# Kernel tuning notes

Hardware: AMD Instinct MI355X
Metric: run time of the kernel (lower is better)

Reference implementation:

```python
import jax, jax.numpy as jnp
import numpy as np

N, F_DIM, H, K, T = 4096, 256, 256, 3, 5
START, END = 10, 3  # args.len_numerical_features, args.num_class


def setup_inputs() -> dict:
    key = jax.random.key(0)
    ks = jax.random.split(key, 8)
    s = 0.05
    x = jax.random.normal(ks[0], (N, F_DIM), dtype=jnp.float32)
    adj = jax.random.randint(ks[1], (N, N, K), 0, 2, dtype=jnp.int32)
    gnn_w = jax.random.normal(ks[2], (K, F_DIM, H), dtype=jnp.float32) * s
    gnn_b = jnp.zeros((K, H), dtype=jnp.float32)
    w_ih = jax.random.normal(ks[3], (K, 4 * H, H), dtype=jnp.float32) * s
    w_hh = jax.random.normal(ks[4], (K, 4 * H, H), dtype=jnp.float32) * s
    b_ih = jnp.zeros((K, 4 * H), dtype=jnp.float32)
    b_hh = jnp.zeros((K, 4 * H), dtype=jnp.float32)
    fc_w = jax.random.normal(ks[5], (K, F_DIM, H), dtype=jnp.float32) * s
    fc_b = jnp.zeros((K, F_DIM), dtype=jnp.float32)
    return dict(x=x, gnn_w=gnn_w, gnn_b=gnn_b, w_ih=w_ih, w_hh=w_hh,
                b_ih=b_ih, b_hh=b_hh, fc_w=fc_w, fc_b=fc_b, adj=adj)


def _gcn(x, a_bin, w, b):
    # PyG GCNConv: A_hat = A + I (self-loops added on top of existing edges,
    # weight 1), out = D^-1/2 A_hat D^-1/2 (x @ W) + b
    a = a_bin + jnp.eye(N, dtype=x.dtype)
    deg = a.sum(axis=1)
    dinv = jnp.where(deg > 0, jax.lax.rsqrt(deg), 0.0)
    a_norm = dinv[:, None] * a * dinv[None, :]
    return a_norm @ (x @ w) + b


def _lstm_last(xt, w_ih, w_hh, b_ih, b_hh):
    # batch_first LSTM over T identical inputs xt [N,H]; returns h at last step
    def step(carry, _):
        h, c = carry
        g = xt @ w_ih.T + b_ih + h @ w_hh.T + b_hh
        i, f, gg, o = jnp.split(g, 4, axis=-1)  # torch gate order: i, f, g, o
        c = jax.nn.sigmoid(f) * c + jax.nn.sigmoid(i) * jnp.tanh(gg)
        h = jax.nn.sigmoid(o) * jnp.tanh(c)
        return (h, c), None
    zero = jnp.zeros((xt.shape[0], H), dtype=xt.dtype)
    (h, c), _ = jax.lax.scan(step, (zero, zero), None, length=T)
    return h


def _sig_slice(z):
    return z.at[:, START:F_DIM - END].set(jax.nn.sigmoid(z[:, START:F_DIM - END]))


def reference(x, gnn_w, gnn_b, w_ih, w_hh, b_ih, b_hh, fc_w, fc_b, adj):
    deltas, zbars = [], []
    for k in range(K):
        a_bin = (adj[:, :, k] != 0).astype(x.dtype)
        # GCN output is identical across timesteps -> compute once
        gnn_out = _gcn(x, a_bin, gnn_w[k], gnn_b[k])
        h_last = _lstm_last(gnn_out, w_ih[k], w_hh[k], b_ih[k], b_hh[k])
        delta = jnp.tanh(h_last @ fc_w[k].T + fc_b[k])  # [N, F]
        deltas.append(delta)
        zbars.append(_sig_slice(x + delta))
    delta_z = jnp.stack(deltas, -1).mean(-1)
    res_z_bar = jnp.stack(zbars, -1)  # [N, F, K]
    pred_matrix = _sig_slice(x + delta_z)
    return pred_matrix, res_z_bar, adj
```

## Files before the change

### kernel.cpp

```cpp
#include <hip/hip_runtime.h>
#include <stdint.h>

#define NN_ 4096
#define FD 256
#define HD 256
#define KC 3
#define GD 1024
#define SA 40
#define BPITCH 144

typedef __attribute__((ext_vector_type(4))) unsigned int vu4;
typedef __attribute__((ext_vector_type(4))) int vi4;
typedef __attribute__((ext_vector_type(4))) float vf4;
typedef __attribute__((ext_vector_type(4))) unsigned short vus4;
typedef __attribute__((ext_vector_type(8))) short short8;
typedef __attribute__((ext_vector_type(4))) float f32x4;

typedef __attribute__((address_space(1))) const void GV;
typedef __attribute__((address_space(3))) void LV;
__device__ __forceinline__ void gl16(const void* g, void* l) {
    __builtin_amdgcn_global_load_lds((GV*)g, (LV*)l, 16, 0, 0);
}

__device__ __forceinline__ float b2f(unsigned short u) {
    unsigned int v = ((unsigned int)u) << 16; float f; __builtin_memcpy(&f, &v, 4); return f;
}
__device__ __forceinline__ unsigned short f2b(float x) {
    unsigned int u; __builtin_memcpy(&u, &x, 4);
    u = (u + 0x7FFFu + ((u >> 16) & 1u)) >> 16;
    return (unsigned short)u;
}
__device__ __forceinline__ void cvt8(const float* __restrict__ g, unsigned short* o) {
    vf4 a = *(const vf4*)g, b = *(const vf4*)(g + 4);
    o[0] = f2b(a[0]); o[1] = f2b(a[1]); o[2] = f2b(a[2]); o[3] = f2b(a[3]);
    o[4] = f2b(b[0]); o[5] = f2b(b[1]); o[6] = f2b(b[2]); o[7] = f2b(b[3]);
}
__device__ __forceinline__ float sigm(float v) { return 1.f / (1.f + __expf(-v)); }

__global__ __launch_bounds__(256) void adj_pass(const int* __restrict__ adj,
        float* __restrict__ adj_out, unsigned char* __restrict__ abits,
        float* __restrict__ dinv,
        const float* __restrict__ wih, const float* __restrict__ whh,
        const float* __restrict__ fcw, unsigned short* __restrict__ wb) {
    const int i = blockIdx.x, t = threadIdx.x;
    if (i < 864) {
        size_t e = ((size_t)i * 256 + t) * 8;
        const float* src; size_t off;
        if (e < 786432)       { src = wih; off = e; }
        else if (e < 1572864) { src = whh; off = e - 786432; }
        else                  { src = fcw; off = e - 1572864; }
        alignas(16) unsigned short o[8];
        cvt8(src + off, o);
        *(vu4*)(wb + e) = *(vu4*)o;
    }
    __shared__ unsigned char nib[3][1024];
    __shared__ float r0[256], r1[256], r2[256];
    const int* src = adj + (size_t)i * 12288;
    float* dstf = adj_out + (size_t)i * 12288;
    float s0 = 0.f, s1 = 0.f, s2 = 0.f;
#pragma unroll
    for (int it = 0; it < 4; ++it) {
        int p = it * 256 + t;
        int jq = p * 4;
        vi4 a = *(const vi4*)(src + jq * 3);
        vi4 b = *(const vi4*)(src + jq * 3 + 4);
        vi4 c = *(const vi4*)(src + jq * 3 + 8);
        int vv[12] = {a[0],a[1],a[2],a[3],b[0],b[1],b[2],b[3],c[0],c[1],c[2],c[3]};
        float ff[12];
#pragma unroll
        for (int e = 0; e < 12; ++e) ff[e] = vv[e] ? 1.f : 0.f;
        vf4 w0 = {ff[0],ff[1],ff[2],ff[3]}, w1 = {ff[4],ff[5],ff[6],ff[7]}, w2 = {ff[8],ff[9],ff[10],ff[11]};
        *(vf4*)(dstf + jq * 3) = w0; *(vf4*)(dstf + jq * 3 + 4) = w1; *(vf4*)(dstf + jq * 3 + 8) = w2;
#pragma unroll
        for (int k = 0; k < 3; ++k) {
            unsigned int nb = (vv[k] ? 1u : 0u) | (vv[3 + k] ? 2u : 0u)
                            | (vv[6 + k] ? 4u : 0u) | (vv[9 + k] ? 8u : 0u);
            nib[k][p] = (unsigned char)nb;
        }
        s0 += ff[0] + ff[3] + ff[6] + ff[9];
        s1 += ff[1] + ff[4] + ff[7] + ff[10];
        s2 += ff[2] + ff[5] + ff[8] + ff[11];
    }
    r0[t] = s0; r1[t] = s1; r2[t] = s2;
    __syncthreads();
#pragma unroll
    for (int k = 0; k < 3; ++k) {
        unsigned int b0 = (unsigned int)nib[k][t * 4 + 0] | ((unsigned int)nib[k][t * 4 + 1] << 4);
        unsigned int b1 = (unsigned int)nib[k][t * 4 + 2] | ((unsigned int)nib[k][t * 4 + 3] << 4);
        *(unsigned short*)(abits + ((size_t)k * NN_ + i) * 512 + t * 2) =
            (unsigned short)(b0 | (b1 << 8));
    }
    for (int off = 128; off > 0; off >>= 1) {
        if (t < off) { r0[t] += r0[t + off]; r1[t] += r1[t + off]; r2[t] += r2[t + off]; }
        __syncthreads();
    }
    if (t == 0) {
        dinv[i]            = 1.f / sqrtf(1.f + r0[0]);
        dinv[NN_ + i]      = 1.f / sqrtf(1.f + r1[0]);
        dinv[2 * NN_ + i]  = 1.f / sqrtf(1.f + r2[0]);
    }
}

__global__ __launch_bounds__(256) void gemm_xw(const float* __restrict__ x,
        const float* __restrict__ gw, const float* __restrict__ dinv,
        unsigned short* __restrict__ yT) {
    __shared__ __align__(16) unsigned short sA[64 * SA], sB[64 * SA];
    const int bi = blockIdx.x, bj = blockIdx.y, k = blockIdx.z;
    const int t = threadIdx.x, lane = t & 63, wave = t >> 6;
    const int m = lane & 15, q = lane >> 4, ko = q * 8;
    const int h0 = bj * 64;
    f32x4 acc[4] = {};
    const float* A0 = x + (size_t)(bi * 64) * FD;
    const float* B0 = gw + (size_t)k * FD * HD;
    const int r = t >> 2, c8 = (t & 3) << 3;
    const int fB = t >> 3, c8B = (t & 7) << 3;
    for (int k0 = 0; k0 < FD; k0 += 32) {
        alignas(16) unsigned short tA[8], tB[8];
        cvt8(A0 + (size_t)r * FD + k0 + c8, tA);
        *(vu4*)(sA + r * SA + c8) = *(vu4*)tA;
        cvt8(B0 + (size_t)(k0 + fB) * HD + h0 + c8B, tB);
#pragma unroll
        for (int e = 0; e < 8; ++e) sB[(c8B + e) * SA + fB] = tB[e];
        __syncthreads();
        short8 af = *(const short8*)(sA + (wave * 16 + m) * SA + ko);
#pragma unroll
        for (int ct = 0; ct < 4; ++ct) {
            short8 bf = *(const short8*)(sB + (ct * 16 + m) * SA + ko);
            acc[ct] = __builtin_amdgcn_mfma_f32_16x16x32_bf16(af, bf, acc[ct], 0, 0, 0);
        }
        __syncthreads();
    }
    unsigned short* yTk = yT + (size_t)k * HD * NN_;
#pragma unroll
    for (int ct = 0; ct < 4; ++ct)
#pragma unroll
        for (int r2 = 0; r2 < 4; ++r2) {
            int col = h0 + ct * 16 + m;
            int row = bi * 64 + wave * 16 + q * 4 + r2;
            yTk[(size_t)col * NN_ + row] = f2b(acc[ct][r2] * dinv[(size_t)k * NN_ + row]);
        }
}

__global__ __launch_bounds__(256) void gemm_agg(const unsigned char* __restrict__ abits,
        const unsigned short* __restrict__ yT, unsigned short* __restrict__ pbuf) {
    __shared__ __align__(16) unsigned char bitsA[128 * BPITCH];
    __shared__ __align__(16) unsigned short sB[128 * 32];
    const int d = blockIdx.x;
    const int w = (d & 7) * 96 + (d >> 3);
    const int bh = w & 1, bi = (w >> 1) & 31, z = w >> 6;
    const int k = z >> 2, s = z & 3;
    const int t = threadIdx.x, lane = t & 63, wave = t >> 6;
    const int wi = wave & 1, wh = wave >> 1;
    const int m = lane & 15, q = lane >> 4, ko = q * 8;
    const int i0 = bi * 128, h0 = bh * 128, jbase = s * 1024;
    {
        const int row = t >> 1, half = t & 1;
        const unsigned char* bsrc = abits + ((size_t)k * NN_ + i0 + row) * 512 + s * 128 + half * 64;
        unsigned char* bdst = bitsA + row * BPITCH + half * 64;
        vu4 v0 = *(const vu4*)(bsrc);
        vu4 v1 = *(const vu4*)(bsrc + 16);
        vu4 v2 = *(const vu4*)(bsrc + 32);
        vu4 v3 = *(const vu4*)(bsrc + 48);
        *(vu4*)(bdst)      = v0;
        *(vu4*)(bdst + 16) = v1;
        *(vu4*)(bdst + 32) = v2;
        *(vu4*)(bdst + 48) = v3;
    }
    f32x4 acc[4][4] = {};
    const int lrow = lane >> 2, lcol = (lane & 3) << 3;
    const unsigned short* Bg0 = yT + ((size_t)(k * 256 + h0 + wave * 32 + lrow)) * NN_ + jbase + lcol;
    const unsigned short* Bg1 = Bg0 + (size_t)16 * NN_;
    unsigned short* lB0 = sB + (wave * 32) * 32;
    unsigned short* lB1 = lB0 + 16 * 32;
    const int arow = (wi * 64 + m) * BPITCH + q;
    for (int j0 = 0; j0 < 1024; j0 += 32) {
        gl16(Bg0 + j0, lB0);
        gl16(Bg1 + j0, lB1);
        __syncthreads();
        const int jby = j0 >> 3;
        short8 af[4], bf[4];
#pragma unroll
        for (int rt = 0; rt < 4; ++rt) {
            unsigned int by = bitsA[arow + rt * 16 * BPITCH + jby];
#pragma unroll
            for (int e = 0; e < 8; ++e)
                af[rt][e] = (short)(((by >> e) & 1u) ? (short)0x3F80 : (short)0);
        }
#pragma unroll
        for (int ct = 0; ct < 4; ++ct)
            bf[ct] = *(const short8*)(sB + (wh * 64 + ct * 16 + m) * 32 + ko);
#pragma unroll
        for (int ct = 0; ct < 4; ++ct)
#pragma unroll
            for (int rt = 0; rt < 4; ++rt)
                acc[rt][ct] = __builtin_amdgcn_mfma_f32_16x16x32_bf16(af[rt], bf[ct], acc[rt][ct], 0, 0, 0);
        __syncthreads();
    }
    const int addself = ((bi >> 3) == s);
#pragma unroll
    for (int rt = 0; rt < 4; ++rt)
#pragma unroll
        for (int ct = 0; ct < 4; ++ct)
#pragma unroll
            for (int r2 = 0; r2 < 4; ++r2) {
                int row = i0 + wi * 64 + rt * 16 + q * 4 + r2;
                int col = h0 + wh * 64 + ct * 16 + m;
                float v = acc[rt][ct][r2];
                if (addself) v += b2f(yT[((size_t)k * 256 + col) * NN_ + row]);
                pbuf[(((size_t)s * 3 + k) * NN_ + row) * 256 + col] = f2b(v);
            }
}

__global__ __launch_bounds__(256) void agg_reduce(const unsigned short* __restrict__ pbuf,
        const float* __restrict__ dinv, const float* __restrict__ gnnb,
        unsigned short* __restrict__ xt) {
    size_t e8 = ((size_t)blockIdx.x * 256 + threadIdx.x) * 8;
    int k = (int)(e8 >> 20);
    int i = (int)((e8 >> 8) & 4095);
    int h = (int)(e8 & 255);
    float di = dinv[k * NN_ + i];
    const size_t KIH = (size_t)KC * NN_ * HD;
    alignas(16) unsigned short p0[8], p1[8], p2[8], p3[8], o[8];
    *(vu4*)p0 = *(const vu4*)(pbuf + 0 * KIH + e8);
    *(vu4*)p1 = *(const vu4*)(pbuf + 1 * KIH + e8);
    *(vu4*)p2 = *(const vu4*)(pbuf + 2 * KIH + e8);
    *(vu4*)p3 = *(const vu4*)(pbuf + 3 * KIH + e8);
#pragma unroll
    for (int e = 0; e < 8; ++e) {
        float v = b2f(p0[e]) + b2f(p1[e]) + b2f(p2[e]) + b2f(p3[e]);
        o[e] = f2b(di * v + gnnb[k * HD + h + e]);
    }
    *(vu4*)(xt + e8) = *(vu4*)o;
}

__global__ __launch_bounds__(256) void lstm_mm(const unsigned short* __restrict__ A,
        const unsigned short* __restrict__ W, const float* __restrict__ b1,
        const float* __restrict__ b2, unsigned short* __restrict__ gX2,
        float* __restrict__ cbuf, unsigned short* __restrict__ hbuf, int mode) {
    __shared__ __align__(16) unsigned short sA[128 * 32];
    __shared__ __align__(16) unsigned short sB[128 * 32];
    const int d = blockIdx.x;
    const int w = (d & 7) * 96 + (d >> 3);
    const int chb = w & 7, bn = w >> 3;
    const int t = threadIdx.x, lane = t & 63, wave = t >> 6;
    const int m = lane & 15, q = lane >> 4, ko = q * 8;
    const int kk = bn >> 5;
    f32x4 acc[2][2][4] = {};
    const int lrow = lane >> 2, lcol = (lane & 3) << 3;
    const unsigned short* A0 = A + (size_t)bn * 128 * 256;
    const unsigned short* W0 = W + (size_t)kk * GD * 256 + (size_t)chb * 32 * 256;
    const unsigned short* Ag0 = A0 + (size_t)(wave * 32 + lrow) * 256 + lcol;
    const unsigned short* Ag1 = Ag0 + 16 * 256;
    const unsigned short* Bg0 = W0 + (size_t)(wave * 256 + lrow) * 256 + lcol;
    const unsigned short* Bg1 = Bg0 + 16 * 256;
    unsigned short* lA0 = sA + (wave * 32) * 32;
    unsigned short* lA1 = lA0 + 16 * 32;
    unsigned short* lB0 = sB + (wave * 32) * 32;
    unsigned short* lB1 = lB0 + 16 * 32;
    for (int k0 = 0; k0 < 256; k0 += 32) {
        gl16(Ag0 + k0, lA0);
        gl16(Ag1 + k0, lA1);
        gl16(Bg0 + k0, lB0);
        gl16(Bg1 + k0, lB1);
        __syncthreads();
        short8 af[2];
#pragma unroll
        for (int rt = 0; rt < 2; ++rt)
            af[rt] = *(const short8*)(sA + (wave * 32 + rt * 16 + m) * 32 + ko);
#pragma unroll
        for (int g = 0; g < 4; ++g)
#pragma unroll
            for (int cc = 0; cc < 2; ++cc) {
                short8 bf = *(const short8*)(sB + (g * 32 + cc * 16 + m) * 32 + ko);
#pragma unroll
                for (int rt = 0; rt < 2; ++rt)
                    acc[rt][cc][g] = __builtin_amdgcn_mfma_f32_16x16x32_bf16(af[rt], bf, acc[rt][cc][g], 0, 0, 0);
            }
        __syncthreads();
    }
#pragma unroll
    for (int rt = 0; rt < 2; ++rt)
#pragma unroll
        for (int cc = 0; cc < 2; ++cc)
#pragma unroll
            for (int r2 = 0; r2 < 4; ++r2) {
                int row = bn * 128 + wave * 32 + rt * 16 + q * 4 + r2;
                int ch = chb * 32 + cc * 16 + m;
                size_t goff = ((size_t)row * 256 + ch) * 4;
                size_t coff = (size_t)row * 256 + ch;
                if (mode == 0) {
                    float v[4];
                    vus4 o;
#pragma unroll
                    for (int g = 0; g < 4; ++g) {
                        v[g] = acc[rt][cc][g][r2]
                             + b1[kk * GD + g * 256 + ch] + b2[kk * GD + g * 256 + ch];
                        o[g] = f2b(v[g]);
                    }
                    *(vus4*)(gX2 + goff) = o;
                    float cn = sigm(v[0]) * tanhf(v[2]);
                    cbuf[coff] = cn;
                    hbuf[coff] = f2b(sigm(v[3]) * tanhf(cn));
                } else {
                    vus4 gv = *(const vus4*)(gX2 + goff);
                    float iv = acc[rt][cc][0][r2] + b2f(gv[0]);
                    float fv = acc[rt][cc][1][r2] + b2f(gv[1]);
                    float gg = acc[rt][cc][2][r2] + b2f(gv[2]);
                    float ov = acc[rt][cc][3][r2] + b2f(gv[3]);
                    float cn = sigm(fv) * cbuf[coff] + sigm(iv) * tanhf(gg);
                    cbuf[coff] = cn;
                    hbuf[coff] = f2b(sigm(ov) * tanhf(cn));
                }
            }
}

__global__ __launch_bounds__(256) void fc_final(const unsigned short* __restrict__ A,
        const unsigned short* __restrict__ W, const float* __restrict__ fcb,
        const float* __restrict__ x, float* __restrict__ pred, float* __restrict__ res) {
    __shared__ __align__(16) unsigned short sA[3][64 * 32], sB[3][64 * 32];
    const int bg = blockIdx.x, bn = blockIdx.y;
    const int t = threadIdx.x, lane = t & 63, wave = t >> 6;
    const int m = lane & 15, q = lane >> 4, ko = q * 8;
    f32x4 acc[3][4] = {};
    const int lrow = lane >> 2, lcol = (lane & 3) << 3;
    const unsigned short* Ag[3]; const unsigned short* Bg[3];
#pragma unroll
    for (int k = 0; k < 3; ++k) {
        Ag[k] = A + ((size_t)k * NN_ + bn * 64 + wave * 16 + lrow) * HD + lcol;
        Bg[k] = W + ((size_t)k * FD + bg * 64 + wave * 16 + lrow) * HD + lcol;
    }
    for (int k0 = 0; k0 < HD; k0 += 32) {
#pragma unroll
        for (int k = 0; k < 3; ++k) {
            gl16(Ag[k] + k0, sA[k] + (wave * 16) * 32);
            gl16(Bg[k] + k0, sB[k] + (wave * 16) * 32);
        }
        __syncthreads();
#pragma unroll
        for (int k = 0; k < 3; ++k) {
            short8 af = *(const short8*)(sA[k] + (wave * 16 + m) * 32 + ko);
#pragma unroll
            for (int ct = 0; ct < 4; ++ct) {
                short8 bf = *(const short8*)(sB[k] + (ct * 16 + m) * 32 + ko);
                acc[k][ct] = __builtin_amdgcn_mfma_f32_16x16x32_bf16(af, bf, acc[k][ct], 0, 0, 0);
            }
        }
        __syncthreads();
    }
#pragma unroll
    for (int ct = 0; ct < 4; ++ct)
#pragma unroll
        for (int r2 = 0; r2 < 4; ++r2) {
            int col = bg * 64 + ct * 16 + m;
            int row = bn * 64 + wave * 16 + q * 4 + r2;
            float d0 = tanhf(acc[0][ct][r2] + fcb[col]);
            float d1 = tanhf(acc[1][ct][r2] + fcb[FD + col]);
            float d2 = tanhf(acc[2][ct][r2] + fcb[2 * FD + col]);
            float xf = x[(size_t)row * FD + col];
            bool sg = (col >= 10) && (col < 253);
            float dm = (d0 + d1 + d2) * (1.f / 3.f);
            float p = xf + dm; if (sg) p = sigm(p);
            pred[(size_t)row * FD + col] = p;
            float z0 = xf + d0; if (sg) z0 = sigm(z0);
            float z1 = xf + d1; if (sg) z1 = sigm(z1);
            float z2 = xf + d2; if (sg) z2 = sigm(z2);
            size_t rb = ((size_t)row * FD + col) * 3;
            res[rb] = z0; res[rb + 1] = z1; res[rb + 2] = z2;
        }
}

extern "C" void kernel_launch(void* const* d_in, const int* in_sizes, int n_in,
                              void* d_out, int out_size, void* d_ws, size_t ws_size,
                              hipStream_t stream) {
    const float* x    = (const float*)d_in[0];
    const float* gnnw = (const float*)d_in[1];
    const float* gnnb = (const float*)d_in[2];
    const float* wih  = (const float*)d_in[3];
    const float* whh  = (const float*)d_in[4];
    const float* bih  = (const float*)d_in[5];
    const float* bhh  = (const float*)d_in[6];
    const float* fcw  = (const float*)d_in[7];
    const float* fcb  = (const float*)d_in[8];
    const int*   adj  = (const int*)d_in[9];

    float* out = (float*)d_out;
    float* out_pred = out;
    float* out_res  = out + (size_t)NN_ * FD;
    float* out_adj  = out + (size_t)NN_ * FD * 4;

    char* ws = (char*)d_ws;
    float*          dinv  = (float*)ws;
    unsigned short* R1    = (unsigned short*)(ws + 49152);
    unsigned short* R2    = (unsigned short*)(ws + 6340608);
    unsigned short* wb    = (unsigned short*)(ws + 12632064);
    unsigned short* pbuf  = (unsigned short*)(ws + 16171008);
    unsigned short* gX2   = pbuf;
    unsigned char*  abits = (unsigned char*)(ws + 41336832);
    float*          cbuf  = (float*)(ws + 47628288);
    const unsigned short* wihb = wb;
    const unsigned short* whhb = wb + 786432;
    const unsigned short* fcwb = wb + 1572864;
    (void)ws_size; (void)in_sizes; (void)n_in; (void)out_size;

    adj_pass<<<dim3(4096), 256, 0, stream>>>(adj, out_adj, abits, dinv, wih, whh, fcw, wb);
    gemm_xw<<<dim3(64, 4, 3), 256, 0, stream>>>(x, gnnw, dinv, R1 );
    gemm_agg<<<dim3(768), 256, 0, stream>>>(abits, R1 , pbuf);
    agg_reduce<<<dim3(1536), 256, 0, stream>>>(pbuf, dinv, gnnb, R2 );
    lstm_mm<<<dim3(768), 256, 0, stream>>>(R2 , wihb, bih, bhh, gX2, cbuf, R1 , 0);
    for (int tstep = 1; tstep < 5; ++tstep)
        lstm_mm<<<dim3(768), 256, 0, stream>>>(R1 , whhb, nullptr, nullptr, gX2, cbuf, R1 , 1);
    fc_final<<<dim3(4, 64), 256, 0, stream>>>(R1 , fcwb, fcb, x, out_pred, out_res);
}
```

Measured before the change: 586.8 us.

## Fuse aggregation reduce into first LSTM GEMM, pre-convert GEMM inputs, widen agg tiles

Folds the split-K partial-sum reduction, normalisation and bias into the A-tile load of the first LSTM input GEMM, which removes the separate agg_reduce kernel and its round trip through memory. x and the transposed GCN weight are converted to bf16 in the adjacency pass, so gemm_xw can use direct global-to-LDS loads. gemm_agg now covers all 256 hidden columns per block (384 blocks), so each adjacency bit tile is expanded once instead of twice, at the cost of higher register pressure. The LSTM steps ping-pong between two hidden buffers, and the workspace is re-laid out so gX2 no longer aliases pbuf.

```diff
diff --git a/kernel.cpp b/kernel.cpp
--- a/kernel.cpp
+++ b/kernel.cpp
@@ -6,7 +6,6 @@
 #define HD 256
 #define KC 3
 #define GD 1024
-#define SA 40
 #define BPITCH 144
 
 typedef __attribute__((ext_vector_type(4))) unsigned int vu4;
@@ -41,17 +40,35 @@
         float* __restrict__ adj_out, unsigned char* __restrict__ abits,
         float* __restrict__ dinv,
         const float* __restrict__ wih, const float* __restrict__ whh,
-        const float* __restrict__ fcw, unsigned short* __restrict__ wb) {
+        const float* __restrict__ fcw, unsigned short* __restrict__ wb,
+        const float* __restrict__ gnnw, const float* __restrict__ x,
+        unsigned short* __restrict__ gwT, unsigned short* __restrict__ xb) {
     const int i = blockIdx.x, t = threadIdx.x;
-    if (i < 864) {
+    if (i < 1472) {
         size_t e = ((size_t)i * 256 + t) * 8;
-        const float* src; size_t off;
-        if (e < 786432)       { src = wih; off = e; }
-        else if (e < 1572864) { src = whh; off = e - 786432; }
-        else                  { src = fcw; off = e - 1572864; }
-        alignas(16) unsigned short o[8];
-        cvt8(src + off, o);
-        *(vu4*)(wb + e) = *(vu4*)o;
+        if (e < 1769472) {
+            const float* src; size_t off;
+            if (e < 786432)       { src = wih; off = e; }
+            else if (e < 1572864) { src = whh; off = e - 786432; }
+            else                  { src = fcw; off = e - 1572864; }
+            alignas(16) unsigned short o[8];
+            cvt8(src + off, o);
+            *(vu4*)(wb + e) = *(vu4*)o;
+        } else if (e < 1966080) {
+            size_t idx = e - 1769472;
+            int k = (int)(idx >> 16), rem = (int)(idx & 65535);
+            int h = rem >> 8, f0 = rem & 255;
+            alignas(16) unsigned short o[8];
+#pragma unroll
+            for (int j = 0; j < 8; ++j)
+                o[j] = f2b(gnnw[((size_t)k * 256 + f0 + j) * 256 + h]);
+            *(vu4*)(gwT + idx) = *(vu4*)o;
+        } else {
+            size_t idx = e - 1966080;
+            alignas(16) unsigned short o[8];
+            cvt8(x + idx, o);
+            *(vu4*)(xb + idx) = *(vu4*)o;
+        }
     }
     __shared__ unsigned char nib[3][1024];
     __shared__ float r0[256], r1[256], r2[256];
@@ -101,31 +118,27 @@
     }
 }
 
-__global__ __launch_bounds__(256) void gemm_xw(const float* __restrict__ x,
-        const float* __restrict__ gw, const float* __restrict__ dinv,
+__global__ __launch_bounds__(256) void gemm_xw(const unsigned short* __restrict__ xb,
+        const unsigned short* __restrict__ gwT, const float* __restrict__ dinv,
         unsigned short* __restrict__ yT) {
-    __shared__ __align__(16) unsigned short sA[64 * SA], sB[64 * SA];
-    const int bi = blockIdx.x, bj = blockIdx.y, k = blockIdx.z;
+    __shared__ __align__(16) unsigned short sA[64 * 32], sB[64 * 32];
+    const int bg = blockIdx.x, bn = blockIdx.y, k = blockIdx.z;
     const int t = threadIdx.x, lane = t & 63, wave = t >> 6;
     const int m = lane & 15, q = lane >> 4, ko = q * 8;
-    const int h0 = bj * 64;
     f32x4 acc[4] = {};
-    const float* A0 = x + (size_t)(bi * 64) * FD;
-    const float* B0 = gw + (size_t)k * FD * HD;
-    const int r = t >> 2, c8 = (t & 3) << 3;
-    const int fB = t >> 3, c8B = (t & 7) << 3;
+    const int lrow = lane >> 2, lcol = (lane & 3) << 3;
+    const unsigned short* Ag = xb + (size_t)(bn * 64 + wave * 16 + lrow) * FD + lcol;
+    const unsigned short* Bg = gwT + (size_t)k * 65536 + (size_t)(bg * 64 + wave * 16 + lrow) * FD + lcol;
+    unsigned short* lA = sA + (wave * 16) * 32;
+    unsigned short* lB = sB + (wave * 16) * 32;
     for (int k0 = 0; k0 < FD; k0 += 32) {
-        alignas(16) unsigned short tA[8], tB[8];
-        cvt8(A0 + (size_t)r * FD + k0 + c8, tA);
-        *(vu4*)(sA + r * SA + c8) = *(vu4*)tA;
-        cvt8(B0 + (size_t)(k0 + fB) * HD + h0 + c8B, tB);
-#pragma unroll
-        for (int e = 0; e < 8; ++e) sB[(c8B + e) * SA + fB] = tB[e];
-        __syncthreads();
-        short8 af = *(const short8*)(sA + (wave * 16 + m) * SA + ko);
+        gl16(Ag + k0, lA);
+        gl16(Bg + k0, lB);
+        __syncthreads();
+        short8 af = *(const short8*)(sA + (wave * 16 + m) * 32 + ko);
 #pragma unroll
         for (int ct = 0; ct < 4; ++ct) {
-            short8 bf = *(const short8*)(sB + (ct * 16 + m) * SA + ko);
+            short8 bf = *(const short8*)(sB + (ct * 16 + m) * 32 + ko);
             acc[ct] = __builtin_amdgcn_mfma_f32_16x16x32_bf16(af, bf, acc[ct], 0, 0, 0);
         }
         __syncthreads();
@@ -135,8 +148,8 @@
     for (int ct = 0; ct < 4; ++ct)
 #pragma unroll
         for (int r2 = 0; r2 < 4; ++r2) {
-            int col = h0 + ct * 16 + m;
-            int row = bi * 64 + wave * 16 + q * 4 + r2;
+            int col = bg * 64 + ct * 16 + m;
+            int row = bn * 64 + wave * 16 + q * 4 + r2;
             yTk[(size_t)col * NN_ + row] = f2b(acc[ct][r2] * dinv[(size_t)k * NN_ + row]);
         }
 }
@@ -144,15 +157,15 @@
 __global__ __launch_bounds__(256) void gemm_agg(const unsigned char* __restrict__ abits,
         const unsigned short* __restrict__ yT, unsigned short* __restrict__ pbuf) {
     __shared__ __align__(16) unsigned char bitsA[128 * BPITCH];
-    __shared__ __align__(16) unsigned short sB[128 * 32];
+    __shared__ __align__(16) unsigned short sB[256 * 32];
     const int d = blockIdx.x;
-    const int w = (d & 7) * 96 + (d >> 3);
-    const int bh = w & 1, bi = (w >> 1) & 31, z = w >> 6;
+    const int w = (d & 7) * 48 + (d >> 3);
+    const int bi = w & 31, z = w >> 5;
     const int k = z >> 2, s = z & 3;
     const int t = threadIdx.x, lane = t & 63, wave = t >> 6;
     const int wi = wave & 1, wh = wave >> 1;
     const int m = lane & 15, q = lane >> 4, ko = q * 8;
-    const int i0 = bi * 128, h0 = bh * 128, jbase = s * 1024;
+    const int i0 = bi * 128, jbase = s * 1024;
     {
         const int row = t >> 1, half = t & 1;
         const unsigned char* bsrc = abits + ((size_t)k * NN_ + i0 + row) * 512 + s * 128 + half * 64;
@@ -166,77 +179,142 @@
         *(vu4*)(bdst + 32) = v2;
         *(vu4*)(bdst + 48) = v3;
     }
-    f32x4 acc[4][4] = {};
+    f32x4 acc[4][8] = {};
     const int lrow = lane >> 2, lcol = (lane & 3) << 3;
-    const unsigned short* Bg0 = yT + ((size_t)(k * 256 + h0 + wave * 32 + lrow)) * NN_ + jbase + lcol;
-    const unsigned short* Bg1 = Bg0 + (size_t)16 * NN_;
-    unsigned short* lB0 = sB + (wave * 32) * 32;
-    unsigned short* lB1 = lB0 + 16 * 32;
-    const int arow = (wi * 64 + m) * BPITCH + q;
+    const unsigned short* Bg[4]; unsigned short* lB[4];
+#pragma unroll
+    for (int v = 0; v < 4; ++v) {
+        Bg[v] = yT + ((size_t)(k * 256 + v * 64 + wave * 16 + lrow)) * NN_ + jbase + lcol;
+        lB[v] = sB + (v * 64 + wave * 16) * 32;
+    }
+    const int arowb = (wi * 64 + m) * BPITCH + q;
     for (int j0 = 0; j0 < 1024; j0 += 32) {
-        gl16(Bg0 + j0, lB0);
-        gl16(Bg1 + j0, lB1);
+#pragma unroll
+        for (int v = 0; v < 4; ++v) gl16(Bg[v] + j0, lB[v]);
         __syncthreads();
         const int jby = j0 >> 3;
-        short8 af[4], bf[4];
+        short8 af[4];
 #pragma unroll
         for (int rt = 0; rt < 4; ++rt) {
-            unsigned int by = bitsA[arow + rt * 16 * BPITCH + jby];
+            unsigned int by = bitsA[arowb + rt * 16 * BPITCH + jby];
 #pragma unroll
             for (int e = 0; e < 8; ++e)
                 af[rt][e] = (short)(((by >> e) & 1u) ? (short)0x3F80 : (short)0);
         }
 #pragma unroll
-        for (int ct = 0; ct < 4; ++ct)
-            bf[ct] = *(const short8*)(sB + (wh * 64 + ct * 16 + m) * 32 + ko);
-#pragma unroll
-        for (int ct = 0; ct < 4; ++ct)
+        for (int ct = 0; ct < 8; ++ct) {
+            short8 bf = *(const short8*)(sB + (wh * 128 + ct * 16 + m) * 32 + ko);
 #pragma unroll
             for (int rt = 0; rt < 4; ++rt)
-                acc[rt][ct] = __builtin_amdgcn_mfma_f32_16x16x32_bf16(af[rt], bf[ct], acc[rt][ct], 0, 0, 0);
+                acc[rt][ct] = __builtin_amdgcn_mfma_f32_16x16x32_bf16(af[rt], bf, acc[rt][ct], 0, 0, 0);
+        }
         __syncthreads();
     }
     const int addself = ((bi >> 3) == s);
 #pragma unroll
     for (int rt = 0; rt < 4; ++rt)
 #pragma unroll
-        for (int ct = 0; ct < 4; ++ct)
+        for (int ct = 0; ct < 8; ++ct)
 #pragma unroll
             for (int r2 = 0; r2 < 4; ++r2) {
                 int row = i0 + wi * 64 + rt * 16 + q * 4 + r2;
-                int col = h0 + wh * 64 + ct * 16 + m;
+                int col = wh * 128 + ct * 16 + m;
                 float v = acc[rt][ct][r2];
                 if (addself) v += b2f(yT[((size_t)k * 256 + col) * NN_ + row]);
                 pbuf[(((size_t)s * 3 + k) * NN_ + row) * 256 + col] = f2b(v);
             }
 }
 
-__global__ __launch_bounds__(256) void agg_reduce(const unsigned short* __restrict__ pbuf,
+__global__ __launch_bounds__(256) void lstm0(const unsigned short* __restrict__ pbuf,
         const float* __restrict__ dinv, const float* __restrict__ gnnb,
-        unsigned short* __restrict__ xt) {
-    size_t e8 = ((size_t)blockIdx.x * 256 + threadIdx.x) * 8;
-    int k = (int)(e8 >> 20);
-    int i = (int)((e8 >> 8) & 4095);
-    int h = (int)(e8 & 255);
-    float di = dinv[k * NN_ + i];
+        const unsigned short* __restrict__ wihb,
+        const float* __restrict__ bih, const float* __restrict__ bhh,
+        unsigned short* __restrict__ gX2, float* __restrict__ cbuf,
+        unsigned short* __restrict__ hout) {
+    __shared__ __align__(16) unsigned short sA[128 * 32];
+    __shared__ __align__(16) unsigned short sB[128 * 32];
+    const int d = blockIdx.x;
+    const int w = (d & 7) * 96 + (d >> 3);
+    const int chb = w & 7, bn = w >> 3;
+    const int t = threadIdx.x, lane = t & 63, wave = t >> 6;
+    const int m = lane & 15, q = lane >> 4, ko = q * 8;
+    const int kk = bn >> 5;
+    f32x4 acc[2][2][4] = {};
+    const int lrow = lane >> 2, lcol = (lane & 3) << 3;
+    const unsigned short* W0 = wihb + (size_t)kk * GD * 256 + (size_t)chb * 32 * 256;
+    const unsigned short* Bg0 = W0 + (size_t)(wave * 256 + lrow) * 256 + lcol;
+    const unsigned short* Bg1 = Bg0 + 16 * 256;
+    unsigned short* lB0 = sB + (wave * 32) * 32;
+    unsigned short* lB1 = lB0 + 16 * 32;
+    const int r = t >> 1, cS = (t & 1) << 4;
+    const int i = (bn & 31) * 128 + r;
+    const float di = dinv[kk * NN_ + i];
+    const size_t prow = ((size_t)kk * NN_ + i) * 256;
     const size_t KIH = (size_t)KC * NN_ * HD;
-    alignas(16) unsigned short p0[8], p1[8], p2[8], p3[8], o[8];
-    *(vu4*)p0 = *(const vu4*)(pbuf + 0 * KIH + e8);
-    *(vu4*)p1 = *(const vu4*)(pbuf + 1 * KIH + e8);
-    *(vu4*)p2 = *(const vu4*)(pbuf + 2 * KIH + e8);
-    *(vu4*)p3 = *(const vu4*)(pbuf + 3 * KIH + e8);
-#pragma unroll
-    for (int e = 0; e < 8; ++e) {
-        float v = b2f(p0[e]) + b2f(p1[e]) + b2f(p2[e]) + b2f(p3[e]);
-        o[e] = f2b(di * v + gnnb[k * HD + h + e]);
-    }
-    *(vu4*)(xt + e8) = *(vu4*)o;
-}
-
-__global__ __launch_bounds__(256) void lstm_mm(const unsigned short* __restrict__ A,
-        const unsigned short* __restrict__ W, const float* __restrict__ b1,
-        const float* __restrict__ b2, unsigned short* __restrict__ gX2,
-        float* __restrict__ cbuf, unsigned short* __restrict__ hbuf, int mode) {
+    for (int k0 = 0; k0 < 256; k0 += 32) {
+        gl16(Bg0 + k0, lB0);
+        gl16(Bg1 + k0, lB1);
+        alignas(16) unsigned short ox[16];
+        const unsigned short* p = pbuf + prow + k0 + cS;
+#pragma unroll
+        for (int hh = 0; hh < 2; ++hh) {
+            alignas(16) unsigned short p0[8], p1[8], p2[8], p3[8];
+            *(vu4*)p0 = *(const vu4*)(p + hh * 8);
+            *(vu4*)p1 = *(const vu4*)(p + KIH + hh * 8);
+            *(vu4*)p2 = *(const vu4*)(p + 2 * KIH + hh * 8);
+            *(vu4*)p3 = *(const vu4*)(p + 3 * KIH + hh * 8);
+#pragma unroll
+            for (int e = 0; e < 8; ++e) {
+                float v = b2f(p0[e]) + b2f(p1[e]) + b2f(p2[e]) + b2f(p3[e]);
+                ox[hh * 8 + e] = f2b(di * v + gnnb[kk * HD + k0 + cS + hh * 8 + e]);
+            }
+        }
+        *(vu4*)(sA + r * 32 + cS)     = *(vu4*)ox;
+        *(vu4*)(sA + r * 32 + cS + 8) = *(vu4*)(ox + 8);
+        __syncthreads();
+        short8 af[2];
+#pragma unroll
+        for (int rt = 0; rt < 2; ++rt)
+            af[rt] = *(const short8*)(sA + (wave * 32 + rt * 16 + m) * 32 + ko);
+#pragma unroll
+        for (int g = 0; g < 4; ++g)
+#pragma unroll
+            for (int cc = 0; cc < 2; ++cc) {
+                short8 bf = *(const short8*)(sB + (g * 32 + cc * 16 + m) * 32 + ko);
+#pragma unroll
+                for (int rt = 0; rt < 2; ++rt)
+                    acc[rt][cc][g] = __builtin_amdgcn_mfma_f32_16x16x32_bf16(af[rt], bf, acc[rt][cc][g], 0, 0, 0);
+            }
+        __syncthreads();
+    }
+#pragma unroll
+    for (int rt = 0; rt < 2; ++rt)
+#pragma unroll
+        for (int cc = 0; cc < 2; ++cc)
+#pragma unroll
+            for (int r2 = 0; r2 < 4; ++r2) {
+                int row = bn * 128 + wave * 32 + rt * 16 + q * 4 + r2;
+                int ch = chb * 32 + cc * 16 + m;
+                size_t goff = ((size_t)row * 256 + ch) * 4;
+                size_t coff = (size_t)row * 256 + ch;
+                float v[4];
+                vus4 o;
+#pragma unroll
+                for (int g = 0; g < 4; ++g) {
+                    v[g] = acc[rt][cc][g][r2]
+                         + bih[kk * GD + g * 256 + ch] + bhh[kk * GD + g * 256 + ch];
+                    o[g] = f2b(v[g]);
+                }
+                *(vus4*)(gX2 + goff) = o;
+                float cn = sigm(v[0]) * tanhf(v[2]);
+                cbuf[coff] = cn;
+                hout[coff] = f2b(sigm(v[3]) * tanhf(cn));
+            }
+}
+
+__global__ __launch_bounds__(256) void lstm_step(const unsigned short* __restrict__ A,
+        const unsigned short* __restrict__ W, const unsigned short* __restrict__ gX2,
+        float* __restrict__ cbuf, unsigned short* __restrict__ hbuf) {
     __shared__ __align__(16) unsigned short sA[128 * 32];
     __shared__ __align__(16) unsigned short sB[128 * 32];
     const int d = blockIdx.x;
@@ -288,29 +366,14 @@
                 int ch = chb * 32 + cc * 16 + m;
                 size_t goff = ((size_t)row * 256 + ch) * 4;
                 size_t coff = (size_t)row * 256 + ch;
-                if (mode == 0) {
-                    float v[4];
-                    vus4 o;
-#pragma unroll
-                    for (int g = 0; g < 4; ++g) {
-                        v[g] = acc[rt][cc][g][r2]
-                             + b1[kk * GD + g * 256 + ch] + b2[kk * GD + g * 256 + ch];
-                        o[g] = f2b(v[g]);
-                    }
-                    *(vus4*)(gX2 + goff) = o;
-                    float cn = sigm(v[0]) * tanhf(v[2]);
-                    cbuf[coff] = cn;
-                    hbuf[coff] = f2b(sigm(v[3]) * tanhf(cn));
-                } else {
-                    vus4 gv = *(const vus4*)(gX2 + goff);
-                    float iv = acc[rt][cc][0][r2] + b2f(gv[0]);
-                    float fv = acc[rt][cc][1][r2] + b2f(gv[1]);
-                    float gg = acc[rt][cc][2][r2] + b2f(gv[2]);
-                    float ov = acc[rt][cc][3][r2] + b2f(gv[3]);
-                    float cn = sigm(fv) * cbuf[coff] + sigm(iv) * tanhf(gg);
-                    cbuf[coff] = cn;
-                    hbuf[coff] = f2b(sigm(ov) * tanhf(cn));
-                }
+                vus4 gv = *(const vus4*)(gX2 + goff);
+                float iv = acc[rt][cc][0][r2] + b2f(gv[0]);
+                float fv = acc[rt][cc][1][r2] + b2f(gv[1]);
+                float gg = acc[rt][cc][2][r2] + b2f(gv[2]);
+                float ov = acc[rt][cc][3][r2] + b2f(gv[3]);
+                float cn = sigm(fv) * cbuf[coff] + sigm(iv) * tanhf(gg);
+                cbuf[coff] = cn;
+                hbuf[coff] = f2b(sigm(ov) * tanhf(cn));
             }
 }
 
@@ -391,23 +454,28 @@
     char* ws = (char*)d_ws;
     float*          dinv  = (float*)ws;
     unsigned short* R1    = (unsigned short*)(ws + 49152);
-    unsigned short* R2    = (unsigned short*)(ws + 6340608);
+    unsigned short* H1    = (unsigned short*)(ws + 6340608);
     unsigned short* wb    = (unsigned short*)(ws + 12632064);
-    unsigned short* pbuf  = (unsigned short*)(ws + 16171008);
-    unsigned short* gX2   = pbuf;
-    unsigned char*  abits = (unsigned char*)(ws + 41336832);
-    float*          cbuf  = (float*)(ws + 47628288);
+    unsigned short* gwT   = (unsigned short*)(ws + 16171008);
+    unsigned short* xb    = (unsigned short*)(ws + 16564224);
+    unsigned char*  abits = (unsigned char*)(ws + 18661376);
+    unsigned short* pbuf  = (unsigned short*)(ws + 24952832);
+    unsigned short* gX2   = (unsigned short*)(ws + 50118656);
+    float*          cbuf  = (float*)(ws + 75284480);
     const unsigned short* wihb = wb;
     const unsigned short* whhb = wb + 786432;
     const unsigned short* fcwb = wb + 1572864;
     (void)ws_size; (void)in_sizes; (void)n_in; (void)out_size;
 
-    adj_pass<<<dim3(4096), 256, 0, stream>>>(adj, out_adj, abits, dinv, wih, whh, fcw, wb);
-    gemm_xw<<<dim3(64, 4, 3), 256, 0, stream>>>(x, gnnw, dinv, R1 );
-    gemm_agg<<<dim3(768), 256, 0, stream>>>(abits, R1 , pbuf);
-    agg_reduce<<<dim3(1536), 256, 0, stream>>>(pbuf, dinv, gnnb, R2 );
-    lstm_mm<<<dim3(768), 256, 0, stream>>>(R2 , wihb, bih, bhh, gX2, cbuf, R1 , 0);
-    for (int tstep = 1; tstep < 5; ++tstep)
-        lstm_mm<<<dim3(768), 256, 0, stream>>>(R1 , whhb, nullptr, nullptr, gX2, cbuf, R1 , 1);
-    fc_final<<<dim3(4, 64), 256, 0, stream>>>(R1 , fcwb, fcb, x, out_pred, out_res);
-}
+    adj_pass<<<dim3(4096), 256, 0, stream>>>(adj, out_adj, abits, dinv,
+                                             wih, whh, fcw, wb, gnnw, x, gwT, xb);
+    gemm_xw<<<dim3(4, 64, 3), 256, 0, stream>>>(xb, gwT, dinv, R1 );
+    gemm_agg<<<dim3(384), 256, 0, stream>>>(abits, R1 , pbuf);
+    lstm0<<<dim3(768), 256, 0, stream>>>(pbuf, dinv, gnnb, wihb, bih, bhh,
+                                         gX2, cbuf, R1);
+    lstm_step<<<dim3(768), 256, 0, stream>>>(R1, whhb, gX2, cbuf, H1);
+    lstm_step<<<dim3(768), 256, 0, stream>>>(H1, whhb, gX2, cbuf, R1);
+    lstm_step<<<dim3(768), 256, 0, stream>>>(R1, whhb, gX2, cbuf, H1);
+    lstm_step<<<dim3(768), 256, 0, stream>>>(H1, whhb, gX2, cbuf, R1);
+    fc_final<<<dim3(4, 64), 256, 0, stream>>>(R1, fcwb, fcb, x, out_pred, out_res);
+}
```

Measured after the change: 616.6 us. +5.1%, slower.

## Fuse x@W GEMM into adjacency pass and fold dinv scaling into aggregation

Applied to the files above, without the earlier changes.

The x@W GEMM moves into the adjacency/weight-conversion kernel as extra blocks, which removes one launch and lets it overlap with the bandwidth-bound adjacency pass. Because dinv is no longer ready when x@W runs, the column-side D^-1/2 scaling moves into the aggregation GEMM: bf16 dinv values replace the constant 1.0 when adjacency bits are expanded, and the self-loop term is scaled explicitly. The LSTM kernel is split into separate gate and step kernels with ping-pong h buffers, so the step kernel no longer reads and writes the same h buffer. This adds extra bf16 rounding of dinv in the aggregation.

```diff
diff --git a/kernel.cpp b/kernel.cpp
--- a/kernel.cpp
+++ b/kernel.cpp
@@ -37,12 +37,56 @@
 }
 __device__ __forceinline__ float sigm(float v) { return 1.f / (1.f + __expf(-v)); }
 
-__global__ __launch_bounds__(256) void adj_pass(const int* __restrict__ adj,
+__global__ __launch_bounds__(256) void adjxw(const int* __restrict__ adj,
         float* __restrict__ adj_out, unsigned char* __restrict__ abits,
-        float* __restrict__ dinv,
+        float* __restrict__ dinv, unsigned short* __restrict__ dinvb,
         const float* __restrict__ wih, const float* __restrict__ whh,
-        const float* __restrict__ fcw, unsigned short* __restrict__ wb) {
-    const int i = blockIdx.x, t = threadIdx.x;
+        const float* __restrict__ fcw, unsigned short* __restrict__ wb,
+        const float* __restrict__ gnnw, const float* __restrict__ x,
+        unsigned short* __restrict__ uT) {
+    const int bid = blockIdx.x, t = threadIdx.x;
+    __shared__ __align__(16) unsigned short sA[64 * SA], sB[64 * SA];
+    __shared__ unsigned char nib[3][1024];
+    __shared__ float r0[256], r1[256], r2[256];
+    if (bid >= 4096) {
+        const int b2 = bid - 4096;
+        const int k = b2 >> 8, rem = b2 & 255, bn = rem >> 2, bg = rem & 3;
+        const int lane = t & 63, wave = t >> 6;
+        const int m = lane & 15, q = lane >> 4, ko = q * 8;
+        const int h0 = bg * 64;
+        f32x4 acc[4] = {};
+        const float* A0 = x + (size_t)(bn * 64) * FD;
+        const float* B0 = gnnw + (size_t)k * FD * HD;
+        const int r = t >> 2, c8 = (t & 3) << 3;
+        const int fB = t >> 3, c8B = (t & 7) << 3;
+        for (int k0 = 0; k0 < FD; k0 += 32) {
+            alignas(16) unsigned short tA[8], tB[8];
+            cvt8(A0 + (size_t)r * FD + k0 + c8, tA);
+            *(vu4*)(sA + r * SA + c8) = *(vu4*)tA;
+            cvt8(B0 + (size_t)(k0 + fB) * HD + h0 + c8B, tB);
+#pragma unroll
+            for (int e = 0; e < 8; ++e) sB[(c8B + e) * SA + fB] = tB[e];
+            __syncthreads();
+            short8 af = *(const short8*)(sA + (wave * 16 + m) * SA + ko);
+#pragma unroll
+            for (int ct = 0; ct < 4; ++ct) {
+                short8 bf = *(const short8*)(sB + (ct * 16 + m) * SA + ko);
+                acc[ct] = __builtin_amdgcn_mfma_f32_16x16x32_bf16(af, bf, acc[ct], 0, 0, 0);
+            }
+            __syncthreads();
+        }
+        unsigned short* uTk = uT + (size_t)k * HD * NN_;
+#pragma unroll
+        for (int ct = 0; ct < 4; ++ct)
+#pragma unroll
+            for (int r2 = 0; r2 < 4; ++r2) {
+                int col = h0 + ct * 16 + m;
+                int row = bn * 64 + wave * 16 + q * 4 + r2;
+                uTk[(size_t)col * NN_ + row] = f2b(acc[ct][r2]);
+            }
+        return;
+    }
+    const int i = bid;
     if (i < 864) {
         size_t e = ((size_t)i * 256 + t) * 8;
         const float* src; size_t off;
@@ -53,8 +97,6 @@
         cvt8(src + off, o);
         *(vu4*)(wb + e) = *(vu4*)o;
     }
-    __shared__ unsigned char nib[3][1024];
-    __shared__ float r0[256], r1[256], r2[256];
     const int* src = adj + (size_t)i * 12288;
     float* dstf = adj_out + (size_t)i * 12288;
     float s0 = 0.f, s1 = 0.f, s2 = 0.f;
@@ -95,56 +137,21 @@
         __syncthreads();
     }
     if (t == 0) {
-        dinv[i]            = 1.f / sqrtf(1.f + r0[0]);
-        dinv[NN_ + i]      = 1.f / sqrtf(1.f + r1[0]);
-        dinv[2 * NN_ + i]  = 1.f / sqrtf(1.f + r2[0]);
-    }
-}
-
-__global__ __launch_bounds__(256) void gemm_xw(const float* __restrict__ x,
-        const float* __restrict__ gw, const float* __restrict__ dinv,
-        unsigned short* __restrict__ yT) {
-    __shared__ __align__(16) unsigned short sA[64 * SA], sB[64 * SA];
-    const int bi = blockIdx.x, bj = blockIdx.y, k = blockIdx.z;
-    const int t = threadIdx.x, lane = t & 63, wave = t >> 6;
-    const int m = lane & 15, q = lane >> 4, ko = q * 8;
-    const int h0 = bj * 64;
-    f32x4 acc[4] = {};
-    const float* A0 = x + (size_t)(bi * 64) * FD;
-    const float* B0 = gw + (size_t)k * FD * HD;
-    const int r = t >> 2, c8 = (t & 3) << 3;
-    const int fB = t >> 3, c8B = (t & 7) << 3;
-    for (int k0 = 0; k0 < FD; k0 += 32) {
-        alignas(16) unsigned short tA[8], tB[8];
-        cvt8(A0 + (size_t)r * FD + k0 + c8, tA);
-        *(vu4*)(sA + r * SA + c8) = *(vu4*)tA;
-        cvt8(B0 + (size_t)(k0 + fB) * HD + h0 + c8B, tB);
-#pragma unroll
-        for (int e = 0; e < 8; ++e) sB[(c8B + e) * SA + fB] = tB[e];
-        __syncthreads();
-        short8 af = *(const short8*)(sA + (wave * 16 + m) * SA + ko);
-#pragma unroll
-        for (int ct = 0; ct < 4; ++ct) {
-            short8 bf = *(const short8*)(sB + (ct * 16 + m) * SA + ko);
-            acc[ct] = __builtin_amdgcn_mfma_f32_16x16x32_bf16(af, bf, acc[ct], 0, 0, 0);
-        }
-        __syncthreads();
-    }
-    unsigned short* yTk = yT + (size_t)k * HD * NN_;
-#pragma unroll
-    for (int ct = 0; ct < 4; ++ct)
-#pragma unroll
-        for (int r2 = 0; r2 < 4; ++r2) {
-            int col = h0 + ct * 16 + m;
-            int row = bi * 64 + wave * 16 + q * 4 + r2;
-            yTk[(size_t)col * NN_ + row] = f2b(acc[ct][r2] * dinv[(size_t)k * NN_ + row]);
-        }
+        float d0 = 1.f / sqrtf(1.f + r0[0]);
+        float d1 = 1.f / sqrtf(1.f + r1[0]);
+        float d2 = 1.f / sqrtf(1.f + r2[0]);
+        dinv[i]           = d0; dinvb[i]            = f2b(d0);
+        dinv[NN_ + i]     = d1; dinvb[NN_ + i]      = f2b(d1);
+        dinv[2 * NN_ + i] = d2; dinvb[2 * NN_ + i]  = f2b(d2);
+    }
 }
 
 __global__ __launch_bounds__(256) void gemm_agg(const unsigned char* __restrict__ abits,
-        const unsigned short* __restrict__ yT, unsigned short* __restrict__ pbuf) {
+        const unsigned short* __restrict__ uT, const unsigned short* __restrict__ dinvb,
+        const float* __restrict__ dinv, unsigned short* __restrict__ pbuf) {
     __shared__ __align__(16) unsigned char bitsA[128 * BPITCH];
     __shared__ __align__(16) unsigned short sB[128 * 32];
+    __shared__ __align__(16) unsigned short sDv[1024];
     const int d = blockIdx.x;
     const int w = (d & 7) * 96 + (d >> 3);
     const int bh = w & 1, bi = (w >> 1) & 31, z = w >> 6;
@@ -166,25 +173,28 @@
         *(vu4*)(bdst + 32) = v2;
         *(vu4*)(bdst + 48) = v3;
     }
+    if (t < 128)
+        *(vu4*)(sDv + t * 8) = *(const vu4*)(dinvb + (size_t)k * NN_ + jbase + t * 8);
     f32x4 acc[4][4] = {};
     const int lrow = lane >> 2, lcol = (lane & 3) << 3;
-    const unsigned short* Bg0 = yT + ((size_t)(k * 256 + h0 + wave * 32 + lrow)) * NN_ + jbase + lcol;
+    const unsigned short* Bg0 = uT + ((size_t)(k * 256 + h0 + wave * 32 + lrow)) * NN_ + jbase + lcol;
     const unsigned short* Bg1 = Bg0 + (size_t)16 * NN_;
     unsigned short* lB0 = sB + (wave * 32) * 32;
     unsigned short* lB1 = lB0 + 16 * 32;
-    const int arow = (wi * 64 + m) * BPITCH + q;
+    const int arowb = (wi * 64 + m) * BPITCH + q;
     for (int j0 = 0; j0 < 1024; j0 += 32) {
         gl16(Bg0 + j0, lB0);
         gl16(Bg1 + j0, lB1);
         __syncthreads();
         const int jby = j0 >> 3;
+        short8 dv = *(const short8*)(sDv + j0 + ko);
         short8 af[4], bf[4];
 #pragma unroll
         for (int rt = 0; rt < 4; ++rt) {
-            unsigned int by = bitsA[arow + rt * 16 * BPITCH + jby];
+            unsigned int by = bitsA[arowb + rt * 16 * BPITCH + jby];
 #pragma unroll
             for (int e = 0; e < 8; ++e)
-                af[rt][e] = (short)(((by >> e) & 1u) ? (short)0x3F80 : (short)0);
+                af[rt][e] = (short)(((by >> e) & 1u) ? dv[e] : (short)0);
         }
 #pragma unroll
         for (int ct = 0; ct < 4; ++ct)
@@ -206,7 +216,9 @@
                 int row = i0 + wi * 64 + rt * 16 + q * 4 + r2;
                 int col = h0 + wh * 64 + ct * 16 + m;
                 float v = acc[rt][ct][r2];
-                if (addself) v += b2f(yT[((size_t)k * 256 + col) * NN_ + row]);
+                if (addself)
+                    v += dinv[(size_t)k * NN_ + row]
+                       * b2f(uT[((size_t)k * 256 + col) * NN_ + row]);
                 pbuf[(((size_t)s * 3 + k) * NN_ + row) * 256 + col] = f2b(v);
             }
 }
@@ -233,10 +245,10 @@
     *(vu4*)(xt + e8) = *(vu4*)o;
 }
 
-__global__ __launch_bounds__(256) void lstm_mm(const unsigned short* __restrict__ A,
+__global__ __launch_bounds__(256) void lstm_gate(const unsigned short* __restrict__ A,
         const unsigned short* __restrict__ W, const float* __restrict__ b1,
         const float* __restrict__ b2, unsigned short* __restrict__ gX2,
-        float* __restrict__ cbuf, unsigned short* __restrict__ hbuf, int mode) {
+        float* __restrict__ cbuf, unsigned short* __restrict__ hbuf) {
     __shared__ __align__(16) unsigned short sA[128 * 32];
     __shared__ __align__(16) unsigned short sB[128 * 32];
     const int d = blockIdx.x;
@@ -288,29 +300,83 @@
                 int ch = chb * 32 + cc * 16 + m;
                 size_t goff = ((size_t)row * 256 + ch) * 4;
                 size_t coff = (size_t)row * 256 + ch;
-                if (mode == 0) {
-                    float v[4];
-                    vus4 o;
-#pragma unroll
-                    for (int g = 0; g < 4; ++g) {
-                        v[g] = acc[rt][cc][g][r2]
-                             + b1[kk * GD + g * 256 + ch] + b2[kk * GD + g * 256 + ch];
-                        o[g] = f2b(v[g]);
-                    }
-                    *(vus4*)(gX2 + goff) = o;
-                    float cn = sigm(v[0]) * tanhf(v[2]);
-                    cbuf[coff] = cn;
-                    hbuf[coff] = f2b(sigm(v[3]) * tanhf(cn));
-                } else {
-                    vus4 gv = *(const vus4*)(gX2 + goff);
-                    float iv = acc[rt][cc][0][r2] + b2f(gv[0]);
-                    float fv = acc[rt][cc][1][r2] + b2f(gv[1]);
-                    float gg = acc[rt][cc][2][r2] + b2f(gv[2]);
-                    float ov = acc[rt][cc][3][r2] + b2f(gv[3]);
-                    float cn = sigm(fv) * cbuf[coff] + sigm(iv) * tanhf(gg);
-                    cbuf[coff] = cn;
-                    hbuf[coff] = f2b(sigm(ov) * tanhf(cn));
+                float v[4];
+                vus4 o;
+#pragma unroll
+                for (int g = 0; g < 4; ++g) {
+                    v[g] = acc[rt][cc][g][r2]
+                         + b1[kk * GD + g * 256 + ch] + b2[kk * GD + g * 256 + ch];
+                    o[g] = f2b(v[g]);
                 }
+                *(vus4*)(gX2 + goff) = o;
+                float cn = sigm(v[0]) * tanhf(v[2]);
+                cbuf[coff] = cn;
+                hbuf[coff] = f2b(sigm(v[3]) * tanhf(cn));
+            }
+}
+
+__global__ __launch_bounds__(256) void lstm_step(const unsigned short* __restrict__ A,
+        const unsigned short* __restrict__ W, const unsigned short* __restrict__ gX2,
+        float* __restrict__ cbuf, unsigned short* __restrict__ hbuf) {
+    __shared__ __align__(16) unsigned short sA[128 * 32];
+    __shared__ __align__(16) unsigned short sB[128 * 32];
+    const int d = blockIdx.x;
+    const int w = (d & 7) * 96 + (d >> 3);
+    const int chb = w & 7, bn = w >> 3;
+    const int t = threadIdx.x, lane = t & 63, wave = t >> 6;
+    const int m = lane & 15, q = lane >> 4, ko = q * 8;
+    const int kk = bn >> 5;
+    f32x4 acc[2][2][4] = {};
+    const int lrow = lane >> 2, lcol = (lane & 3) << 3;
+    const unsigned short* A0 = A + (size_t)bn * 128 * 256;
+    const unsigned short* W0 = W + (size_t)kk * GD * 256 + (size_t)chb * 32 * 256;
+    const unsigned short* Ag0 = A0 + (size_t)(wave * 32 + lrow) * 256 + lcol;
+    const unsigned short* Ag1 = Ag0 + 16 * 256;
+    const unsigned short* Bg0 = W0 + (size_t)(wave * 256 + lrow) * 256 + lcol;
+    const unsigned short* Bg1 = Bg0 + 16 * 256;
+    unsigned short* lA0 = sA + (wave * 32) * 32;
+    unsigned short* lA1 = lA0 + 16 * 32;
+    unsigned short* lB0 = sB + (wave * 32) * 32;
+    unsigned short* lB1 = lB0 + 16 * 32;
+    for (int k0 = 0; k0 < 256; k0 += 32) {
+        gl16(Ag0 + k0, lA0);
+        gl16(Ag1 + k0, lA1);
+        gl16(Bg0 + k0, lB0);
+        gl16(Bg1 + k0, lB1);
+        __syncthreads();
+        short8 af[2];
+#pragma unroll
+        for (int rt = 0; rt < 2; ++rt)
+            af[rt] = *(const short8*)(sA + (wave * 32 + rt * 16 + m) * 32 + ko);
+#pragma unroll
+        for (int g = 0; g < 4; ++g)
+#pragma unroll
+            for (int cc = 0; cc < 2; ++cc) {
+                short8 bf = *(const short8*)(sB + (g * 32 + cc * 16 + m) * 32 + ko);
+#pragma unroll
+                for (int rt = 0; rt < 2; ++rt)
+                    acc[rt][cc][g] = __builtin_amdgcn_mfma_f32_16x16x32_bf16(af[rt], bf, acc[rt][cc][g], 0, 0, 0);
+            }
+        __syncthreads();
+    }
+#pragma unroll
+    for (int rt = 0; rt < 2; ++rt)
+#pragma unroll
+        for (int cc = 0; cc < 2; ++cc)
+#pragma unroll
+            for (int r2 = 0; r2 < 4; ++r2) {
+                int row = bn * 128 + wave * 32 + rt * 16 + q * 4 + r2;
+                int ch = chb * 32 + cc * 16 + m;
+                size_t goff = ((size_t)row * 256 + ch) * 4;
+                size_t coff = (size_t)row * 256 + ch;
+                vus4 gv = *(const vus4*)(gX2 + goff);
+                float iv = acc[rt][cc][0][r2] + b2f(gv[0]);
+                float fv = acc[rt][cc][1][r2] + b2f(gv[1]);
+                float gg = acc[rt][cc][2][r2] + b2f(gv[2]);
+                float ov = acc[rt][cc][3][r2] + b2f(gv[3]);
+                float cn = sigm(fv) * cbuf[coff] + sigm(iv) * tanhf(gg);
+                cbuf[coff] = cn;
+                hbuf[coff] = f2b(sigm(ov) * tanhf(cn));
             }
 }
 
@@ -390,24 +456,28 @@
 
     char* ws = (char*)d_ws;
     float*          dinv  = (float*)ws;
-    unsigned short* R1    = (unsigned short*)(ws + 49152);
-    unsigned short* R2    = (unsigned short*)(ws + 6340608);
-    unsigned short* wb    = (unsigned short*)(ws + 12632064);
-    unsigned short* pbuf  = (unsigned short*)(ws + 16171008);
-    unsigned short* gX2   = pbuf;
-    unsigned char*  abits = (unsigned char*)(ws + 41336832);
-    float*          cbuf  = (float*)(ws + 47628288);
+    unsigned short* dinvb = (unsigned short*)(ws + 49152);
+    unsigned short* R1    = (unsigned short*)(ws + 73728);
+    unsigned short* H1    = (unsigned short*)(ws + 6365184);
+    unsigned short* XT    = (unsigned short*)(ws + 12656640);
+    unsigned short* wb    = (unsigned short*)(ws + 18948096);
+    unsigned char*  abits = (unsigned char*)(ws + 22487040);
+    unsigned short* pbuf  = (unsigned short*)(ws + 28778496);
+    unsigned short* gX2   = (unsigned short*)(ws + 53944320);
+    float*          cbuf  = (float*)(ws + 79110144);
     const unsigned short* wihb = wb;
     const unsigned short* whhb = wb + 786432;
     const unsigned short* fcwb = wb + 1572864;
     (void)ws_size; (void)in_sizes; (void)n_in; (void)out_size;
 
-    adj_pass<<<dim3(4096), 256, 0, stream>>>(adj, out_adj, abits, dinv, wih, whh, fcw, wb);
-    gemm_xw<<<dim3(64, 4, 3), 256, 0, stream>>>(x, gnnw, dinv, R1 );
-    gemm_agg<<<dim3(768), 256, 0, stream>>>(abits, R1 , pbuf);
-    agg_reduce<<<dim3(1536), 256, 0, stream>>>(pbuf, dinv, gnnb, R2 );
-    lstm_mm<<<dim3(768), 256, 0, stream>>>(R2 , wihb, bih, bhh, gX2, cbuf, R1 , 0);
-    for (int tstep = 1; tstep < 5; ++tstep)
-        lstm_mm<<<dim3(768), 256, 0, stream>>>(R1 , whhb, nullptr, nullptr, gX2, cbuf, R1 , 1);
-    fc_final<<<dim3(4, 64), 256, 0, stream>>>(R1 , fcwb, fcb, x, out_pred, out_res);
-}
+    adjxw<<<dim3(4864), 256, 0, stream>>>(adj, out_adj, abits, dinv, dinvb,
+                                          wih, whh, fcw, wb, gnnw, x, R1 );
+    gemm_agg<<<dim3(768), 256, 0, stream>>>(abits, R1 , dinvb, dinv, pbuf);
+    agg_reduce<<<dim3(1536), 256, 0, stream>>>(pbuf, dinv, gnnb, XT);
+    lstm_gate<<<dim3(768), 256, 0, stream>>>(XT, wihb, bih, bhh, gX2, cbuf, R1);
+    lstm_step<<<dim3(768), 256, 0, stream>>>(R1, whhb, gX2, cbuf, H1);
+    lstm_step<<<dim3(768), 256, 0, stream>>>(H1, whhb, gX2, cbuf, R1);
+    lstm_step<<<dim3(768), 256, 0, stream>>>(R1, whhb, gX2, cbuf, H1);
+    lstm_step<<<dim3(768), 256, 0, stream>>>(H1, whhb, gX2, cbuf, R1);
+    fc_final<<<dim3(4, 64), 256, 0, stream>>>(R1, fcwb, fcb, x, out_pred, out_res);
+}
```

After: 580.4 us. About the same (-1.1%).
